# Kernel optimization log

Measured on AMD Instinct MI355X. Metric: run time of the kernel, lower is better.

The kernel has to match this reference:

```python
import jax, jax.numpy as jnp
import numpy as np
from itertools import product

DIM = 384
HEADS = 8
DIM_HEAD = 64
INNER = HEADS * DIM_HEAD  # 512
KS = 3                    # kernel_size (attention window)
PAD = KS // 2
W_WIN = KS * KS           # 9
SCALE = DIM_HEAD ** -0.5


def setup_inputs() -> dict:
    key = jax.random.key(0)
    k1, k2, k3, k4, k5 = jax.random.split(key, 5)
    B, H, W = 4, 56, 56
    x = jax.random.normal(k1, (B, DIM, H, W), dtype=jnp.float32)
    # 1x1 conv weights stored as (out_ch, in_ch)
    Wq = jax.random.normal(k2, (INNER, DIM), dtype=jnp.float32) * (DIM ** -0.5)
    Wkv = jax.random.normal(k3, (2 * INNER, DIM), dtype=jnp.float32) * (DIM ** -0.5)
    Wo = jax.random.normal(k4, (DIM, INNER), dtype=jnp.float32) * (INNER ** -0.5)
    bo = jax.random.normal(k5, (DIM,), dtype=jnp.float32) * 0.01
    return {"x": x, "Wq": Wq, "Wkv": Wkv, "Wo": Wo, "bo": bo}


def _conv1x1(x, w):
    # x: (B,Cin,H,W), w: (Cout,Cin) -> (B,Cout,H,W)
    return jnp.einsum('bchw,oc->bohw', x, w)


def reference(x, Wq, Wkv, Wo, bo):
    B, C, H, W = x.shape
    q = _conv1x1(x, Wq)                       # (B, INNER, H, W)
    kv = _conv1x1(x, Wkv)                     # (B, 2*INNER, H, W)
    k, v = jnp.split(kv, 2, axis=1)
    # split channels heads-major, matching torch reshape (B, heads, dh, H, W)
    q = q.reshape(B, HEADS, DIM_HEAD, H, W)
    k = k.reshape(B, HEADS, DIM_HEAD, H, W)
    v = v.reshape(B, HEADS, DIM_HEAD, H, W)
    # zero-pad spatial dims (matches F.unfold zero padding: padded taps get logit 0)
    k_pad = jnp.pad(k, ((0, 0), (0, 0), (0, 0), (PAD, PAD), (PAD, PAD)))
    v_pad = jnp.pad(v, ((0, 0), (0, 0), (0, 0), (PAD, PAD), (PAD, PAD)))
    offsets = list(product(range(KS), range(KS)))  # row-major = unfold order
    # dots: (B, heads, H, W, w)
    dots = jnp.stack([
        jnp.einsum('bhdxy,bhdxy->bhxy', q, k_pad[:, :, :, i:i + H, j:j + W])
        for (i, j) in offsets
    ], axis=-1) * SCALE
    attn = jax.nn.softmax(dots, axis=-1)      # softmax over the 9-tap window
    # weighted sum of shifted v: (B, heads, dh, H, W)
    out = sum(
        attn[:, :, None, :, :, w_idx] * v_pad[:, :, :, i:i + H, j:j + W]
        for w_idx, (i, j) in enumerate(offsets)
    )
    out = out.reshape(B, INNER, H, W)
    return _conv1x1(out, Wo) + bo[None, :, None, None]
```

## Files before the change

### kernel.cpp

```cpp
#include <hip/hip_runtime.h>


#define HW 3136
#define WIMG 56
#define QKV_CH 1536
#define SCALE 0.125f
#define KSTR 72
#define NROWS 242
#define QKV_T 6422528

typedef __bf16 bf16x8_t __attribute__((ext_vector_type(8)));
typedef float f32x4_t __attribute__((ext_vector_type(4)));
typedef unsigned short ushort8 __attribute__((ext_vector_type(8)));

__device__ __forceinline__ float bf2f(unsigned short u) {
    return __uint_as_float(((unsigned int)u) << 16);
}
__device__ __forceinline__ unsigned short f2bf(float f) {
    unsigned int u = __float_as_uint(f);
    u += 0x7FFFu + ((u >> 16) & 1u);
    return (unsigned short)(u >> 16);
}

__device__ __forceinline__ void gll16(const unsigned short* g, unsigned short* l) {
    __builtin_amdgcn_global_load_lds(
        (const __attribute__((address_space(1))) unsigned int*)g,
        (__attribute__((address_space(3))) unsigned int*)l,
        16, 0, 0);
}

__global__ __launch_bounds__(256) void cvt_all(
    const float* __restrict__ x,
    const float* __restrict__ Wq, const float* __restrict__ Wkv,
    const float* __restrict__ Wo,
    unsigned short* __restrict__ xT,
    unsigned short* __restrict__ wT, unsigned short* __restrict__ wT3)
{
    __shared__ unsigned short Tl[64 * 36];
    const int bx = blockIdx.x;
    const int t = threadIdx.x;

    if (bx < 2400) {
        const int sblk = bx % 50;
        const int kblk = (bx / 50) % 12;
        const int b    = bx / 600;

        if (sblk == 49) {
            unsigned short* dst = xT + (((size_t)b * 25 + 24) * 12 + kblk) * 4096 + 2048;
            *reinterpret_cast<uint4*>(dst + t * 8) = (uint4){0, 0, 0, 0};
            return;
        }

        const float* xp = x + ((size_t)b * 384 + (size_t)kblk * 32) * HW + sblk * 64;
        const int c = t >> 3;
#pragma unroll
        for (int i = 0; i < 2; i++) {
            const int sc = (t & 7) + 8 * i;
            const float4 v = *reinterpret_cast<const float4*>(xp + (size_t)c * HW + sc * 4);
            const int s4 = sc * 4;
            Tl[(s4 + 0) * 36 + c] = f2bf(v.x);
            Tl[(s4 + 1) * 36 + c] = f2bf(v.y);
            Tl[(s4 + 2) * 36 + c] = f2bf(v.z);
            Tl[(s4 + 3) * 36 + c] = f2bf(v.w);
        }
        __syncthreads();

        const int row = t >> 2, gran = t & 3;
        const uint2 lo = *reinterpret_cast<const uint2*>(&Tl[row * 36 + gran * 8]);
        const uint2 hi = *reinterpret_cast<const uint2*>(&Tl[row * 36 + gran * 8 + 4]);
        uint4 o; o.x = lo.x; o.y = lo.y; o.z = hi.x; o.w = hi.y;
        unsigned short* dst = xT + (((size_t)b * 25 + (sblk >> 1)) * 12 + kblk) * 4096
                            + (sblk & 1) * 2048;
        *reinterpret_cast<uint4*>(dst + t * 8) = o;
        return;
    }

    const int i = (bx - 2400) * 256 + t;
    if (i < 73728) {
        const int g = i & 3;
        const int idx3 = i >> 2;
        const int o128 = idx3 & 127;
        const int rest = idx3 >> 7;
        const int kb = rest % 12, oblk = rest / 12;
        const int o = oblk * 128 + o128;
        const int k0 = kb * 32 + g * 8;
        const float* src = (o < 512) ? (Wq + (size_t)o * 384 + k0)
                                     : (Wkv + (size_t)(o - 512) * 384 + k0);
        const float4 v0 = *reinterpret_cast<const float4*>(src);
        const float4 v1 = *reinterpret_cast<const float4*>(src + 4);
        uint4 u;
        u.x = (unsigned int)f2bf(v0.x) | ((unsigned int)f2bf(v0.y) << 16);
        u.y = (unsigned int)f2bf(v0.z) | ((unsigned int)f2bf(v0.w) << 16);
        u.z = (unsigned int)f2bf(v1.x) | ((unsigned int)f2bf(v1.y) << 16);
        u.w = (unsigned int)f2bf(v1.z) | ((unsigned int)f2bf(v1.w) << 16);
        reinterpret_cast<uint4*>(wT)[i] = u;
    } else {
        const int j = i - 73728;
        const int g = j & 3;
        const int idx3 = j >> 2;
        const int o128 = idx3 & 127;
        const int rest = idx3 >> 7;
        const int kb = rest % 16, oblk = rest / 16;
        const int o = oblk * 128 + o128;
        const float* src = Wo + (size_t)o * 512 + kb * 32 + g * 8;
        const float4 v0 = *reinterpret_cast<const float4*>(src);
        const float4 v1 = *reinterpret_cast<const float4*>(src + 4);
        uint4 u;
        u.x = (unsigned int)f2bf(v0.x) | ((unsigned int)f2bf(v0.y) << 16);
        u.y = (unsigned int)f2bf(v0.z) | ((unsigned int)f2bf(v0.w) << 16);
        u.z = (unsigned int)f2bf(v1.x) | ((unsigned int)f2bf(v1.y) << 16);
        u.w = (unsigned int)f2bf(v1.z) | ((unsigned int)f2bf(v1.w) << 16);
        reinterpret_cast<uint4*>(wT3)[j] = u;
    }
}

__global__ __launch_bounds__(256) void gemm1(
    const unsigned short* __restrict__ xT,
    const unsigned short* __restrict__ wT,
    unsigned short* __restrict__ qkvT)
{
    __shared__ __align__(16) unsigned short A_lds[128 * 32];
    __shared__ __align__(16) unsigned short B_lds[128 * 32];

    const int sblk = blockIdx.x;
    const int oblk = blockIdx.y;
    const int b  = blockIdx.z;
    const int t  = threadIdx.x;
    const int lane = t & 63, w = t >> 6;
    const int quad = lane >> 4, mrow = lane & 15;
    const int wm = w >> 1, wn = w & 1;

    const unsigned short* wsrc = wT + ((size_t)oblk * 12) * 4096;
    const unsigned short* xsrc = xT + (((size_t)b * 25 + sblk) * 12) * 4096;

    f32x4_t acc[4][4];
#pragma unroll
    for (int m = 0; m < 4; m++)
#pragma unroll
        for (int n = 0; n < 4; n++) acc[m][n] = (f32x4_t){0.f, 0.f, 0.f, 0.f};

    for (int kb = 0; kb < 12; kb++) {
        __syncthreads();
        gll16(wsrc + (size_t)kb * 4096 + t * 8,        A_lds + t * 8);
        gll16(wsrc + (size_t)kb * 4096 + 2048 + t * 8, A_lds + 2048 + t * 8);
        gll16(xsrc + (size_t)kb * 4096 + t * 8,        B_lds + t * 8);
        gll16(xsrc + (size_t)kb * 4096 + 2048 + t * 8, B_lds + 2048 + t * 8);
        __syncthreads();

        bf16x8_t af[4], bf[4];
#pragma unroll
        for (int m = 0; m < 4; m++)
            af[m] = *reinterpret_cast<const bf16x8_t*>(&A_lds[(wm * 64 + m * 16 + mrow) * 32 + quad * 8]);
#pragma unroll
        for (int n = 0; n < 4; n++)
            bf[n] = *reinterpret_cast<const bf16x8_t*>(&B_lds[(wn * 64 + n * 16 + mrow) * 32 + quad * 8]);
#pragma unroll
        for (int m = 0; m < 4; m++)
#pragma unroll
            for (int n = 0; n < 4; n++)
                acc[m][n] = __builtin_amdgcn_mfma_f32_16x16x32_bf16(af[m], bf[n], acc[m][n], 0, 0, 0);
    }

    const int which = oblk >> 2;
    const int hq = (oblk & 3) * 2 + wm;
    const int s0 = sblk * 128 + wn * 64;
    unsigned short* outb = qkvT + (size_t)which * QKV_T
                         + ((size_t)(b * 8 + hq) * HW) * 64;
#pragma unroll
    for (int m = 0; m < 4; m++) {
        const int d0 = m * 16 + quad * 4;
#pragma unroll
        for (int n = 0; n < 4; n++) {
            const int ss = s0 + n * 16 + mrow;
            if (ss < HW) {
                uint2 u;
                u.x = (unsigned int)f2bf(acc[m][n][0]) | ((unsigned int)f2bf(acc[m][n][1]) << 16);
                u.y = (unsigned int)f2bf(acc[m][n][2]) | ((unsigned int)f2bf(acc[m][n][3]) << 16);
                *reinterpret_cast<uint2*>(outb + (size_t)ss * 64 + d0) = u;
            }
        }
    }
}

__global__ __launch_bounds__(256) void natt2(
    const unsigned short* __restrict__ qkvT,
    unsigned short* __restrict__ aoT)
{
    __shared__ __align__(16) unsigned short KV[NROWS * KSTR];
    __shared__ float dred[9 * 2 * 128];

    const int t = threadIdx.x;
    const int p  = t & 127;
    const int dq = t >> 7;
    const int sblk = blockIdx.x;
    const int s0 = sblk * 128;
    const int s  = s0 + p;
    const int h  = blockIdx.y, b = blockIdx.z;
    const int sc = min(s, HW - 1);
    const int y  = sc / WIMG, xx = sc % WIMG;

    const unsigned short* qg = qkvT + ((size_t)(b * 8 + h) * HW) * 64;
    const unsigned short* kg = qg + (size_t)QKV_T;
    const unsigned short* vg = qg + (size_t)(2 * QKV_T);

#pragma unroll
    for (int i = 0; i < 8; i++) {
        const int f = i * 256 + t;
        if (f < NROWS * 8) {
            const int row = f >> 3, c8 = f & 7;
            int srow = s0 - 57 + row;
            srow = min(max(srow, 0), HW - 1);
            const uint4 k4 = *reinterpret_cast<const uint4*>(kg + (size_t)srow * 64 + c8 * 8);
            *reinterpret_cast<uint4*>(&KV[row * KSTR + c8 * 8]) = k4;
        }
    }

    int   roff[9];
    float msk[9];
#pragma unroll
    for (int ty = 0; ty < 3; ty++)
#pragma unroll
        for (int tx = 0; tx < 3; tx++) {
            const int tap = ty * 3 + tx;
            const int ny = y + ty - 1, nx = xx + tx - 1;
            const bool v = (ny >= 0) && (ny < WIMG) && (nx >= 0) && (nx < WIMG);
            roff[tap] = (v ? ((ty - 1) * WIMG + (tx - 1)) : 0) * KSTR;
            msk[tap]  = v ? 1.f : 0.f;
        }

    float qv[32];
#pragma unroll
    for (int c = 0; c < 4; c++) {
        const uint4 q4 = *reinterpret_cast<const uint4*>(qg + (size_t)sc * 64 + dq * 32 + c * 8);
        qv[c*8+0] = bf2f((unsigned short)(q4.x & 0xffff)); qv[c*8+1] = bf2f((unsigned short)(q4.x >> 16));
        qv[c*8+2] = bf2f((unsigned short)(q4.y & 0xffff)); qv[c*8+3] = bf2f((unsigned short)(q4.y >> 16));
        qv[c*8+4] = bf2f((unsigned short)(q4.z & 0xffff)); qv[c*8+5] = bf2f((unsigned short)(q4.z >> 16));
        qv[c*8+6] = bf2f((unsigned short)(q4.w & 0xffff)); qv[c*8+7] = bf2f((unsigned short)(q4.w >> 16));
    }

    __syncthreads();

    const int rbase = (57 + p) * KSTR + dq * 32;

    float dots[9];
#pragma unroll
    for (int tp = 0; tp < 9; tp++) dots[tp] = 0.f;
#pragma unroll
    for (int ch = 0; ch < 4; ch++) {
#pragma unroll
        for (int tp = 0; tp < 9; tp++) {
            const ushort8 kk = *reinterpret_cast<const ushort8*>(&KV[rbase + roff[tp] + ch * 8]);
#pragma unroll
            for (int j = 0; j < 8; j++)
                dots[tp] += qv[ch * 8 + j] * bf2f(kk[j]);
        }
    }

    __syncthreads();

#pragma unroll
    for (int tp = 0; tp < 9; tp++) dred[(tp * 2 + dq) * 128 + p] = dots[tp];
#pragma unroll
    for (int i = 0; i < 8; i++) {
        const int f = i * 256 + t;
        if (f < NROWS * 8) {
            const int row = f >> 3, c8 = f & 7;
            int srow = s0 - 57 + row;
            srow = min(max(srow, 0), HW - 1);
            const uint4 v4 = *reinterpret_cast<const uint4*>(vg + (size_t)srow * 64 + c8 * 8);
            *reinterpret_cast<uint4*>(&KV[row * KSTR + c8 * 8]) = v4;
        }
    }

    __syncthreads();

    float mx = -1e30f, dt[9];
#pragma unroll
    for (int tp = 0; tp < 9; tp++) {
        const float sum = dred[(tp * 2 + 0) * 128 + p] + dred[(tp * 2 + 1) * 128 + p];
        dt[tp] = msk[tp] * (sum * SCALE);
        mx = fmaxf(mx, dt[tp]);
    }
    float se = 0.f, w9[9];
#pragma unroll
    for (int tp = 0; tp < 9; tp++) { w9[tp] = __expf(dt[tp] - mx); se += w9[tp]; }
    const float inv = 1.f / se;
#pragma unroll
    for (int tp = 0; tp < 9; tp++) w9[tp] *= inv * msk[tp];

    float o[32];
#pragma unroll
    for (int dd = 0; dd < 32; dd++) o[dd] = 0.f;
#pragma unroll
    for (int ch = 0; ch < 4; ch++) {
        ushort8 vfr[9];
#pragma unroll
        for (int tp = 0; tp < 9; tp++)
            vfr[tp] = *reinterpret_cast<const ushort8*>(&KV[rbase + roff[tp] + ch * 8]);
#pragma unroll
        for (int j = 0; j < 8; j++)
#pragma unroll
            for (int tp = 0; tp < 9; tp++)
                o[ch * 8 + j] += w9[tp] * bf2f(vfr[tp][j]);
    }

    if (s < HW) {
        __align__(16) unsigned short ov[32];
#pragma unroll
        for (int dd = 0; dd < 32; dd++) ov[dd] = f2bf(o[dd]);
        unsigned short* dst = aoT + (((size_t)(b * 49 + (s >> 6))) * 16 + (h * 2 + dq)) * 2048
                            + (s & 63) * 32;
        *reinterpret_cast<uint4*>(dst)      = *reinterpret_cast<const uint4*>(ov);
        *reinterpret_cast<uint4*>(dst + 8)  = *reinterpret_cast<const uint4*>(ov + 8);
        *reinterpret_cast<uint4*>(dst + 16) = *reinterpret_cast<const uint4*>(ov + 16);
        *reinterpret_cast<uint4*>(dst + 24) = *reinterpret_cast<const uint4*>(ov + 24);
    }
}

__global__ __launch_bounds__(256) void gemm3(
    const unsigned short* __restrict__ aoT,
    const unsigned short* __restrict__ wT3,
    const float* __restrict__ bias,
    float* __restrict__ out)
{
    __shared__ __align__(16) unsigned short A_lds[128 * 32];
    __shared__ __align__(16) unsigned short B_lds[64 * 32];

    const int sblk = blockIdx.x;
    const int oblk = blockIdx.y;
    const int b  = blockIdx.z;
    const int t  = threadIdx.x;
    const int lane = t & 63, w = t >> 6;
    const int quad = lane >> 4, mrow = lane & 15;
    const int wm = w >> 1, wn = w & 1;

    const unsigned short* asrc = wT3 + (size_t)oblk * 16 * 4096;
    const unsigned short* bsrc = aoT + ((size_t)(b * 49 + sblk)) * 16 * 2048;

    f32x4_t acc[4][2];
#pragma unroll
    for (int m = 0; m < 4; m++)
#pragma unroll
        for (int n = 0; n < 2; n++) acc[m][n] = (f32x4_t){0.f, 0.f, 0.f, 0.f};

    for (int kb = 0; kb < 16; kb++) {
        __syncthreads();
        gll16(asrc + (size_t)kb * 4096 + t * 8,        A_lds + t * 8);
        gll16(asrc + (size_t)kb * 4096 + 2048 + t * 8, A_lds + 2048 + t * 8);
        gll16(bsrc + (size_t)kb * 2048 + t * 8,        B_lds + t * 8);
        __syncthreads();

        bf16x8_t af[4], bf[2];
#pragma unroll
        for (int m = 0; m < 4; m++)
            af[m] = *reinterpret_cast<const bf16x8_t*>(&A_lds[(wm * 64 + m * 16 + mrow) * 32 + quad * 8]);
#pragma unroll
        for (int n = 0; n < 2; n++)
            bf[n] = *reinterpret_cast<const bf16x8_t*>(&B_lds[(wn * 32 + n * 16 + mrow) * 32 + quad * 8]);
#pragma unroll
        for (int m = 0; m < 4; m++)
#pragma unroll
            for (int n = 0; n < 2; n++)
                acc[m][n] = __builtin_amdgcn_mfma_f32_16x16x32_bf16(af[m], bf[n], acc[m][n], 0, 0, 0);
    }

    const int o0 = oblk * 128 + wm * 64;
    const int s0 = sblk * 64 + wn * 32;
    float* outb = out + (size_t)b * 384 * HW;
#pragma unroll
    for (int m = 0; m < 4; m++)
#pragma unroll
        for (int n = 0; n < 2; n++) {
            const int ss = s0 + n * 16 + mrow;
#pragma unroll
            for (int r = 0; r < 4; r++) {
                const int oo = o0 + m * 16 + quad * 4 + r;
                outb[(size_t)oo * HW + ss] = acc[m][n][r] + bias[oo];
            }
        }
}

extern "C" void kernel_launch(void* const* d_in, const int* in_sizes, int n_in,
                              void* d_out, int out_size, void* d_ws, size_t ws_size,
                              hipStream_t stream) {
    const float* x   = (const float*)d_in[0];
    const float* Wq  = (const float*)d_in[1];
    const float* Wkv = (const float*)d_in[2];
    const float* Wo  = (const float*)d_in[3];
    const float* bo  = (const float*)d_in[4];
    float* out = (float*)d_out;

    unsigned short* xT   = (unsigned short*)d_ws;
    unsigned short* wT   = xT + (size_t)4915200;
    unsigned short* wT3  = wT + (size_t)589824;
    unsigned short* qkvT = wT3 + (size_t)196608;
    unsigned short* aoT  = qkvT + (size_t)(3 * QKV_T);

    cvt_all<<<dim3(2784), 256, 0, stream>>>(x, Wq, Wkv, Wo, xT, wT, wT3);

    gemm1<<<dim3(25, 12, 4), 256, 0, stream>>>(xT, wT, qkvT);
    natt2<<<dim3(25, 8, 4), 256, 0, stream>>>(qkvT, aoT);
    gemm3<<<dim3(49, 3, 4), 256, 0, stream>>>(aoT, wT3, bo, out);
}
```

Before: 141.1 us.

## Load two K-slices per barrier in GEMMs and swizzle block order for XCD locality

gemm1 and gemm3 now stage two 32-wide K slices per sync pair instead of one, halving the number of barriers and issuing more global-to-LDS loads in flight per iteration. gemm1 and natt2 switch to a 1-D grid with an 8-way swizzle, so consecutive blocks landing on the same XCD share nearby tiles and get better L2 reuse. The cost is doubled LDS per block, which may lower occupancy, and it is not true double buffering, since loads and compute still do not overlap.

```diff
diff --git a/kernel.cpp b/kernel.cpp
--- a/kernel.cpp
+++ b/kernel.cpp
@@ -119,12 +119,15 @@
     const unsigned short* __restrict__ wT,
     unsigned short* __restrict__ qkvT)
 {
-    __shared__ __align__(16) unsigned short A_lds[128 * 32];
-    __shared__ __align__(16) unsigned short B_lds[128 * 32];
-
-    const int sblk = blockIdx.x;
-    const int oblk = blockIdx.y;
-    const int b  = blockIdx.z;
+    __shared__ __align__(16) unsigned short A_lds[2][128 * 32];
+    __shared__ __align__(16) unsigned short B_lds[2][128 * 32];
+
+    const int lin = blockIdx.x;
+    const int swz = (lin & 7) * 150 + (lin >> 3);
+    const int sblk = swz % 25;
+    const int oblk = (swz / 25) % 12;
+    const int b    = swz / 300;
+
     const int t  = threadIdx.x;
     const int lane = t & 63, w = t >> 6;
     const int quad = lane >> 4, mrow = lane & 15;
@@ -139,26 +142,35 @@
 #pragma unroll
         for (int n = 0; n < 4; n++) acc[m][n] = (f32x4_t){0.f, 0.f, 0.f, 0.f};
 
-    for (int kb = 0; kb < 12; kb++) {
+    for (int kb = 0; kb < 6; kb++) {
+        const size_t k0 = (size_t)(2 * kb) * 4096;
+        const size_t k1 = (size_t)(2 * kb + 1) * 4096;
         __syncthreads();
-        gll16(wsrc + (size_t)kb * 4096 + t * 8,        A_lds + t * 8);
-        gll16(wsrc + (size_t)kb * 4096 + 2048 + t * 8, A_lds + 2048 + t * 8);
-        gll16(xsrc + (size_t)kb * 4096 + t * 8,        B_lds + t * 8);
-        gll16(xsrc + (size_t)kb * 4096 + 2048 + t * 8, B_lds + 2048 + t * 8);
+        gll16(wsrc + k0 + t * 8,        A_lds[0] + t * 8);
+        gll16(wsrc + k0 + 2048 + t * 8, A_lds[0] + 2048 + t * 8);
+        gll16(wsrc + k1 + t * 8,        A_lds[1] + t * 8);
+        gll16(wsrc + k1 + 2048 + t * 8, A_lds[1] + 2048 + t * 8);
+        gll16(xsrc + k0 + t * 8,        B_lds[0] + t * 8);
+        gll16(xsrc + k0 + 2048 + t * 8, B_lds[0] + 2048 + t * 8);
+        gll16(xsrc + k1 + t * 8,        B_lds[1] + t * 8);
+        gll16(xsrc + k1 + 2048 + t * 8, B_lds[1] + 2048 + t * 8);
         __syncthreads();
 
-        bf16x8_t af[4], bf[4];
-#pragma unroll
-        for (int m = 0; m < 4; m++)
-            af[m] = *reinterpret_cast<const bf16x8_t*>(&A_lds[(wm * 64 + m * 16 + mrow) * 32 + quad * 8]);
-#pragma unroll
-        for (int n = 0; n < 4; n++)
-            bf[n] = *reinterpret_cast<const bf16x8_t*>(&B_lds[(wn * 64 + n * 16 + mrow) * 32 + quad * 8]);
-#pragma unroll
-        for (int m = 0; m < 4; m++)
+#pragma unroll
+        for (int ks = 0; ks < 2; ks++) {
+            bf16x8_t af[4], bfr[4];
+#pragma unroll
+            for (int m = 0; m < 4; m++)
+                af[m] = *reinterpret_cast<const bf16x8_t*>(&A_lds[ks][(wm * 64 + m * 16 + mrow) * 32 + quad * 8]);
 #pragma unroll
             for (int n = 0; n < 4; n++)
-                acc[m][n] = __builtin_amdgcn_mfma_f32_16x16x32_bf16(af[m], bf[n], acc[m][n], 0, 0, 0);
+                bfr[n] = *reinterpret_cast<const bf16x8_t*>(&B_lds[ks][(wn * 64 + n * 16 + mrow) * 32 + quad * 8]);
+#pragma unroll
+            for (int m = 0; m < 4; m++)
+#pragma unroll
+                for (int n = 0; n < 4; n++)
+                    acc[m][n] = __builtin_amdgcn_mfma_f32_16x16x32_bf16(af[m], bfr[n], acc[m][n], 0, 0, 0);
+        }
     }
 
     const int which = oblk >> 2;
@@ -189,13 +201,17 @@
     __shared__ __align__(16) unsigned short KV[NROWS * KSTR];
     __shared__ float dred[9 * 2 * 128];
 
+    const int lin = blockIdx.x;
+    const int swz = (lin & 7) * 100 + (lin >> 3);
+    const int sblk = swz % 25;
+    const int h = (swz / 25) & 7;
+    const int b = swz / 200;
+
     const int t = threadIdx.x;
     const int p  = t & 127;
     const int dq = t >> 7;
-    const int sblk = blockIdx.x;
     const int s0 = sblk * 128;
     const int s  = s0 + p;
-    const int h  = blockIdx.y, b = blockIdx.z;
     const int sc = min(s, HW - 1);
     const int y  = sc / WIMG, xx = sc % WIMG;
 
@@ -323,8 +339,8 @@
     const float* __restrict__ bias,
     float* __restrict__ out)
 {
-    __shared__ __align__(16) unsigned short A_lds[128 * 32];
-    __shared__ __align__(16) unsigned short B_lds[64 * 32];
+    __shared__ __align__(16) unsigned short A_lds[2][128 * 32];
+    __shared__ __align__(16) unsigned short B_lds[2][64 * 32];
 
     const int sblk = blockIdx.x;
     const int oblk = blockIdx.y;
@@ -343,25 +359,35 @@
 #pragma unroll
         for (int n = 0; n < 2; n++) acc[m][n] = (f32x4_t){0.f, 0.f, 0.f, 0.f};
 
-    for (int kb = 0; kb < 16; kb++) {
+    for (int kb = 0; kb < 8; kb++) {
+        const size_t a0 = (size_t)(2 * kb) * 4096;
+        const size_t a1 = (size_t)(2 * kb + 1) * 4096;
+        const size_t b0 = (size_t)(2 * kb) * 2048;
+        const size_t b1 = (size_t)(2 * kb + 1) * 2048;
         __syncthreads();
-        gll16(asrc + (size_t)kb * 4096 + t * 8,        A_lds + t * 8);
-        gll16(asrc + (size_t)kb * 4096 + 2048 + t * 8, A_lds + 2048 + t * 8);
-        gll16(bsrc + (size_t)kb * 2048 + t * 8,        B_lds + t * 8);
+        gll16(asrc + a0 + t * 8,        A_lds[0] + t * 8);
+        gll16(asrc + a0 + 2048 + t * 8, A_lds[0] + 2048 + t * 8);
+        gll16(asrc + a1 + t * 8,        A_lds[1] + t * 8);
+        gll16(asrc + a1 + 2048 + t * 8, A_lds[1] + 2048 + t * 8);
+        gll16(bsrc + b0 + t * 8,        B_lds[0] + t * 8);
+        gll16(bsrc + b1 + t * 8,        B_lds[1] + t * 8);
         __syncthreads();
 
-        bf16x8_t af[4], bf[2];
-#pragma unroll
-        for (int m = 0; m < 4; m++)
-            af[m] = *reinterpret_cast<const bf16x8_t*>(&A_lds[(wm * 64 + m * 16 + mrow) * 32 + quad * 8]);
-#pragma unroll
-        for (int n = 0; n < 2; n++)
-            bf[n] = *reinterpret_cast<const bf16x8_t*>(&B_lds[(wn * 32 + n * 16 + mrow) * 32 + quad * 8]);
-#pragma unroll
-        for (int m = 0; m < 4; m++)
+#pragma unroll
+        for (int ks = 0; ks < 2; ks++) {
+            bf16x8_t af[4], bfr[2];
+#pragma unroll
+            for (int m = 0; m < 4; m++)
+                af[m] = *reinterpret_cast<const bf16x8_t*>(&A_lds[ks][(wm * 64 + m * 16 + mrow) * 32 + quad * 8]);
 #pragma unroll
             for (int n = 0; n < 2; n++)
-                acc[m][n] = __builtin_amdgcn_mfma_f32_16x16x32_bf16(af[m], bf[n], acc[m][n], 0, 0, 0);
+                bfr[n] = *reinterpret_cast<const bf16x8_t*>(&B_lds[ks][(wn * 32 + n * 16 + mrow) * 32 + quad * 8]);
+#pragma unroll
+            for (int m = 0; m < 4; m++)
+#pragma unroll
+                for (int n = 0; n < 2; n++)
+                    acc[m][n] = __builtin_amdgcn_mfma_f32_16x16x32_bf16(af[m], bfr[n], acc[m][n], 0, 0, 0);
+        }
     }
 
     const int o0 = oblk * 128 + wm * 64;
@@ -398,7 +424,7 @@
 
     cvt_all<<<dim3(2784), 256, 0, stream>>>(x, Wq, Wkv, Wo, xT, wT, wT3);
 
-    gemm1<<<dim3(25, 12, 4), 256, 0, stream>>>(xT, wT, qkvT);
-    natt2<<<dim3(25, 8, 4), 256, 0, stream>>>(qkvT, aoT);
+    gemm1<<<dim3(1200), 256, 0, stream>>>(xT, wT, qkvT);
+    natt2<<<dim3(800), 256, 0, stream>>>(qkvT, aoT);
     gemm3<<<dim3(49, 3, 4), 256, 0, stream>>>(aoT, wT3, bo, out);
 }
```

Result: faster. 135.0 us (-4.3%).
